# Kernel optimization log

Hardware: AMD Instinct MI355X
Metric: run time of the kernel (lower is better)

Reference implementation:

```python
import jax, jax.numpy as jnp
import numpy as np

B, S, D = 1024, 192, 512
MAX_ITEMS, NUM_LAYERS = 64, 3
LN_EPS = 1e-5


def setup_inputs() -> dict:
    key = jax.random.key(0)
    k_tok, k_pad, k_item, k_layer, k_temp = jax.random.split(key, 5)
    token_embeddings = jax.random.normal(k_tok, (B, S, D), dtype=jnp.float32)
    # Left-padded mask: zeros then contiguous ones until the end of the row.
    pad_len = jax.random.randint(k_pad, (B,), 0, S)  # at least 1 real token
    attention_mask = (jnp.arange(S)[None, :] >= pad_len[:, None]).astype(jnp.int32)
    item_pos_emb = 0.01 * jax.random.normal(k_item, (MAX_ITEMS, D), dtype=jnp.float32)
    layer_emb = 0.01 * jax.random.normal(k_layer, (NUM_LAYERS, D), dtype=jnp.float32)
    temporal_decay = 0.02 * jax.random.normal(k_temp, (MAX_ITEMS, D), dtype=jnp.float32)
    ln_weight = jnp.ones((D,), dtype=jnp.float32)
    ln_bias = jnp.zeros((D,), dtype=jnp.float32)
    return {
        "token_embeddings": token_embeddings,
        "attention_mask": attention_mask,
        "item_pos_emb": item_pos_emb,
        "layer_emb": layer_emb,
        "temporal_decay": temporal_decay,
        "ln_weight": ln_weight,
        "ln_bias": ln_bias,
    }


def reference(token_embeddings, attention_mask, item_pos_emb, layer_emb,
              temporal_decay, ln_weight, ln_bias):
    mask = attention_mask > 0                              # (B, S) bool
    has_content = jnp.any(mask, axis=1)                    # (B,)
    start = jnp.argmax(mask, axis=1)                       # first non-pad index
    end = S - jnp.argmax(mask[:, ::-1], axis=1)            # last non-pad index + 1
    idx = jnp.arange(S)[None, :]                           # (1, S)
    pos = idx - start[:, None]                             # content-relative position
    in_range = (pos >= 0) & (idx < end[:, None]) & has_content[:, None]
    pos_c = jnp.clip(pos, 0)
    item_idx = jnp.where(in_range, pos_c // NUM_LAYERS, 0)  # (B, S)
    layer_idx = jnp.where(in_range, pos_c % NUM_LAYERS, 0)
    add = item_pos_emb[item_idx] + layer_emb[layer_idx] + temporal_decay[item_idx]
    enhanced = token_embeddings + jnp.where(in_range[..., None], add, 0.0)
    # LayerNorm over last dim
    mu = jnp.mean(enhanced, axis=-1, keepdims=True)
    var = jnp.mean(jnp.square(enhanced - mu), axis=-1, keepdims=True)
    normed = (enhanced - mu) * jax.lax.rsqrt(var + LN_EPS) * ln_weight + ln_bias
    # zero out padding (dropout is identity in eval mode)
    return normed * attention_mask[..., None].astype(normed.dtype)
```

## Files before the change

kernel.cpp:

```cpp
#include <hip/hip_runtime.h>

typedef float f4 __attribute__((ext_vector_type(4)));

#define BB 1024
#define SS 192
#define DD 512
#define NUM_LAYERS 3
#define LN_EPS 1e-5f

__global__ __launch_bounds__(256) void prep_kernel(
    const int* __restrict__ mask,
    const float* __restrict__ item_pos,
    const float* __restrict__ layer_emb,
    const float* __restrict__ decay,
    float* __restrict__ add_tab,
    int* __restrict__ start)
{
    if (blockIdx.x < SS) {
        const int p = blockIdx.x;
        const int t = threadIdx.x;
        if (t < DD / 4) {
            const int item = p / NUM_LAYERS;
            const int layer = p - item * NUM_LAYERS;
            const f4 iv = reinterpret_cast<const f4*>(item_pos + item * DD)[t];
            const f4 lv = reinterpret_cast<const f4*>(layer_emb + layer * DD)[t];
            const f4 dv = reinterpret_cast<const f4*>(decay + item * DD)[t];
            reinterpret_cast<f4*>(add_tab + p * DD)[t] = iv + lv + dv;
        }
    } else {
        const int b = (blockIdx.x - SS) * 4 + (threadIdx.x >> 6);
        const int lane = threadIdx.x & 63;
        if (b < BB) {
            const int* m = mask + b * SS;
            const unsigned long long b0 = __ballot(m[lane] > 0);
            const unsigned long long b1 = __ballot(m[lane + 64] > 0);
            const unsigned long long b2 = __ballot(m[lane + 128] > 0);
            int idx;
            if (b0)      idx = __ffsll(b0) - 1;
            else if (b1) idx = 64 + __ffsll(b1) - 1;
            else if (b2) idx = 128 + __ffsll(b2) - 1;
            else         idx = SS;
            if (lane == 0) start[b] = idx;
        }
    }
}

__device__ __forceinline__ float wave_allreduce(float v, int xaddr32) {
    v += __uint_as_float((unsigned)__builtin_amdgcn_update_dpp(
            0, (int)__float_as_uint(v), 0xB1, 0xF, 0xF, true));
    v += __uint_as_float((unsigned)__builtin_amdgcn_update_dpp(
            0, (int)__float_as_uint(v), 0x4E, 0xF, 0xF, true));
    v += __uint_as_float((unsigned)__builtin_amdgcn_update_dpp(
            0, (int)__float_as_uint(v), 0x141, 0xF, 0xF, true));
    v += __uint_as_float((unsigned)__builtin_amdgcn_update_dpp(
            0, (int)__float_as_uint(v), 0x140, 0xF, 0xF, true));
    v += __uint_as_float((unsigned)__builtin_amdgcn_ds_swizzle(
            (int)__float_as_uint(v), 0x401f));
    v += __uint_as_float((unsigned)__builtin_amdgcn_ds_bpermute(
            xaddr32, (int)__float_as_uint(v)));
    return v;
}

__global__ __launch_bounds__(256) void fused_kernel(
    const float* __restrict__ tok,
    const float* __restrict__ add_tab,
    const float* __restrict__ lnw,
    const float* __restrict__ lnb,
    const int* __restrict__ start,
    float* __restrict__ out)
{
    const int b = blockIdx.x >> 1;
    const int half = blockIdx.x & 1;
    const int tid = threadIdx.x;
    const int wid = tid >> 6;
    const int lane = tid & 63;
    const int l0 = lane;
    const int l1 = lane + 64;
    const int xaddr32 = (lane ^ 32) << 2;

    const int st = start[b];

    const f4 w0 = reinterpret_cast<const f4*>(lnw)[l0];
    const f4 w1 = reinterpret_cast<const f4*>(lnw)[l1];
    const f4 c0 = reinterpret_cast<const f4*>(lnb)[l0];
    const f4 c1 = reinterpret_cast<const f4*>(lnb)[l1];

    float* const obase = out + (size_t)b * SS * DD;

    {
        f4* o4 = reinterpret_cast<f4*>(obase);
        const int nf4 = st * (DD / 4);
        const f4 z = {0.f, 0.f, 0.f, 0.f};
        for (int i = half * 256 + tid; i < nf4; i += 512)
            o4[i] = z;
    }

    const int j = half * 4 + wid;

    #pragma unroll 1
    for (int s = st + j; s < SS; s += 8) {
        const int pos = s - st;

        const f4* x4 = reinterpret_cast<const f4*>(tok + (size_t)b * SS * DD + s * DD);
        const f4 xv0 = x4[l0];
        const f4 xv1 = x4[l1];

        const f4* a4 = reinterpret_cast<const f4*>(add_tab + pos * DD);
        const f4 y0 = xv0 + a4[l0];
        const f4 y1 = xv1 + a4[l1];

        float sum = (y0.x + y0.y) + (y0.z + y0.w)
                  + (y1.x + y1.y) + (y1.z + y1.w);
        const f4 q0 = y0 * y0;
        const f4 q1 = y1 * y1;
        float sq = (q0.x + q0.y) + (q0.z + q0.w)
                 + (q1.x + q1.y) + (q1.z + q1.w);

        sum = wave_allreduce(sum, xaddr32);
        sq  = wave_allreduce(sq, xaddr32);

        const float mu  = sum * (1.0f / DD);
        const float var = sq * (1.0f / DD) - mu * mu;
        const float inv = rsqrtf(var + LN_EPS);

        f4* o4 = reinterpret_cast<f4*>(obase + s * DD);
        o4[l0] = (y0 - mu) * inv * w0 + c0;
        o4[l1] = (y1 - mu) * inv * w1 + c1;
    }
}

extern "C" void kernel_launch(void* const* d_in, const int* in_sizes, int n_in,
                              void* d_out, int out_size, void* d_ws, size_t ws_size,
                              hipStream_t stream) {
    const float* tok       = (const float*)d_in[0];
    const int*   mask      = (const int*)d_in[1];
    const float* item_pos  = (const float*)d_in[2];
    const float* layer_emb = (const float*)d_in[3];
    const float* decay     = (const float*)d_in[4];
    const float* lnw       = (const float*)d_in[5];
    const float* lnb       = (const float*)d_in[6];
    float* out = (float*)d_out;

    float* add_tab = (float*)d_ws;
    int* start = (int*)((char*)d_ws + (size_t)SS * DD * sizeof(float));

    prep_kernel<<<SS + 256, 256, 0, stream>>>(mask, item_pos, layer_emb, decay,
                                              add_tab, start);
    fused_kernel<<<BB * 2, 256, 0, stream>>>(tok, add_tab, lnw, lnb, start, out);
}
```

Baseline: 148.7 us.

## Split zero-fill into separate kernel and grid-stride content rows across global waves

Moves the padding zero-fill and start-index computation into a dedicated kernel, and reworks the LayerNorm kernel into a persistent grid-stride loop over all B*S rows, where each wave skips rows that are padding. The aim is to balance work across waves regardless of how much padding each batch row has, since the old per-batch mapping gave uneven loads. In exchange it adds a third kernel launch, extra passes over the mask, and iterations in which waves only skip pad rows.

```diff
diff --git a/kernel.cpp b/kernel.cpp
--- a/kernel.cpp
+++ b/kernel.cpp
@@ -7,42 +7,53 @@
 #define DD 512
 #define NUM_LAYERS 3
 #define LN_EPS 1e-5f
+#define NROWS (BB * SS)
+#define CONTENT_BLOCKS 2048
+#define NWAVES (CONTENT_BLOCKS * 4)
 
-__global__ __launch_bounds__(256) void prep_kernel(
+__global__ __launch_bounds__(256) void zerofill_kernel(
     const int* __restrict__ mask,
+    int* __restrict__ start,
+    float* __restrict__ out)
+{
+    const int b = blockIdx.x >> 1;
+    const int half = blockIdx.x & 1;
+    const int tid = threadIdx.x;
+    const int lane = tid & 63;
+
+    const int* m = mask + b * SS;
+    const unsigned long long b0 = __ballot(m[lane] > 0);
+    const unsigned long long b1 = __ballot(m[lane + 64] > 0);
+    const unsigned long long b2 = __ballot(m[lane + 128] > 0);
+    int st;
+    if (b0)      st = __ffsll(b0) - 1;
+    else if (b1) st = 64 + __ffsll(b1) - 1;
+    else if (b2) st = 128 + __ffsll(b2) - 1;
+    else         st = SS;
+
+    if (half == 0 && tid == 0) start[b] = st;
+
+    f4* o4 = reinterpret_cast<f4*>(out + (size_t)b * SS * DD);
+    const int nf4 = st * (DD / 4);
+    const f4 z = {0.f, 0.f, 0.f, 0.f};
+    for (int i = half * 256 + tid; i < nf4; i += 512)
+        o4[i] = z;
+}
+
+__global__ __launch_bounds__(128) void prep_kernel(
     const float* __restrict__ item_pos,
     const float* __restrict__ layer_emb,
     const float* __restrict__ decay,
-    float* __restrict__ add_tab,
-    int* __restrict__ start)
+    float* __restrict__ add_tab)
 {
-    if (blockIdx.x < SS) {
-        const int p = blockIdx.x;
-        const int t = threadIdx.x;
-        if (t < DD / 4) {
-            const int item = p / NUM_LAYERS;
-            const int layer = p - item * NUM_LAYERS;
-            const f4 iv = reinterpret_cast<const f4*>(item_pos + item * DD)[t];
-            const f4 lv = reinterpret_cast<const f4*>(layer_emb + layer * DD)[t];
-            const f4 dv = reinterpret_cast<const f4*>(decay + item * DD)[t];
-            reinterpret_cast<f4*>(add_tab + p * DD)[t] = iv + lv + dv;
-        }
-    } else {
-        const int b = (blockIdx.x - SS) * 4 + (threadIdx.x >> 6);
-        const int lane = threadIdx.x & 63;
-        if (b < BB) {
-            const int* m = mask + b * SS;
-            const unsigned long long b0 = __ballot(m[lane] > 0);
-            const unsigned long long b1 = __ballot(m[lane + 64] > 0);
-            const unsigned long long b2 = __ballot(m[lane + 128] > 0);
-            int idx;
-            if (b0)      idx = __ffsll(b0) - 1;
-            else if (b1) idx = 64 + __ffsll(b1) - 1;
-            else if (b2) idx = 128 + __ffsll(b2) - 1;
-            else         idx = SS;
-            if (lane == 0) start[b] = idx;
-        }
-    }
+    const int p = blockIdx.x;
+    const int t = threadIdx.x;
+    const int item = p / NUM_LAYERS;
+    const int layer = p - item * NUM_LAYERS;
+    const f4 iv = reinterpret_cast<const f4*>(item_pos + item * DD)[t];
+    const f4 lv = reinterpret_cast<const f4*>(layer_emb + layer * DD)[t];
+    const f4 dv = reinterpret_cast<const f4*>(decay + item * DD)[t];
+    reinterpret_cast<f4*>(add_tab + p * DD)[t] = iv + lv + dv;
 }
 
 __device__ __forceinline__ float wave_allreduce(float v, int xaddr32) {
@@ -61,7 +72,7 @@
     return v;
 }
 
-__global__ __launch_bounds__(256) void fused_kernel(
+__global__ __launch_bounds__(256) void content_kernel(
     const float* __restrict__ tok,
     const float* __restrict__ add_tab,
     const float* __restrict__ lnw,
@@ -69,39 +80,30 @@
     const int* __restrict__ start,
     float* __restrict__ out)
 {
-    const int b = blockIdx.x >> 1;
-    const int half = blockIdx.x & 1;
-    const int tid = threadIdx.x;
-    const int wid = tid >> 6;
-    const int lane = tid & 63;
+    const int wid = threadIdx.x >> 6;
+    const int lane = threadIdx.x & 63;
     const int l0 = lane;
     const int l1 = lane + 64;
     const int xaddr32 = (lane ^ 32) << 2;
-
-    const int st = start[b];
 
     const f4 w0 = reinterpret_cast<const f4*>(lnw)[l0];
     const f4 w1 = reinterpret_cast<const f4*>(lnw)[l1];
     const f4 c0 = reinterpret_cast<const f4*>(lnb)[l0];
     const f4 c1 = reinterpret_cast<const f4*>(lnb)[l1];
 
-    float* const obase = out + (size_t)b * SS * DD;
-
-    {
-        f4* o4 = reinterpret_cast<f4*>(obase);
-        const int nf4 = st * (DD / 4);
-        const f4 z = {0.f, 0.f, 0.f, 0.f};
-        for (int i = half * 256 + tid; i < nf4; i += 512)
-            o4[i] = z;
-    }
-
-    const int j = half * 4 + wid;
+    const int wave = blockIdx.x * 4 + wid;
 
     #pragma unroll 1
-    for (int s = st + j; s < SS; s += 8) {
+    for (int row = wave; row < NROWS; row += NWAVES) {
+        const int b = row / SS;
+        const int s = row - b * SS;
+        const int st = start[b];
+
+        if (s < st) continue;
+
         const int pos = s - st;
 
-        const f4* x4 = reinterpret_cast<const f4*>(tok + (size_t)b * SS * DD + s * DD);
+        const f4* x4 = reinterpret_cast<const f4*>(tok + (size_t)row * DD);
         const f4 xv0 = x4[l0];
         const f4 xv1 = x4[l1];
 
@@ -123,7 +125,7 @@
         const float var = sq * (1.0f / DD) - mu * mu;
         const float inv = rsqrtf(var + LN_EPS);
 
-        f4* o4 = reinterpret_cast<f4*>(obase + s * DD);
+        f4* o4 = reinterpret_cast<f4*>(out + (size_t)row * DD);
         o4[l0] = (y0 - mu) * inv * w0 + c0;
         o4[l1] = (y1 - mu) * inv * w1 + c1;
     }
@@ -144,7 +146,8 @@
     float* add_tab = (float*)d_ws;
     int* start = (int*)((char*)d_ws + (size_t)SS * DD * sizeof(float));
 
-    prep_kernel<<<SS + 256, 256, 0, stream>>>(mask, item_pos, layer_emb, decay,
-                                              add_tab, start);
-    fused_kernel<<<BB * 2, 256, 0, stream>>>(tok, add_tab, lnw, lnb, start, out);
+    zerofill_kernel<<<BB * 2, 256, 0, stream>>>(mask, start, out);
+    prep_kernel<<<SS, 128, 0, stream>>>(item_pos, layer_emb, decay, add_tab);
+    content_kernel<<<CONTENT_BLOCKS, 256, 0, stream>>>(tok, add_tab, lnw, lnb,
+                                                       start, out);
 }
```

Measured after the change: 153.1 us. 1.03x slower.
